# Kernel optimization log

Measured on AMD Instinct MI355X. Metric: run time of the kernel, lower is better.

Reference implementation:

```python
import jax, jax.numpy as jnp
import numpy as np

NUM_CAPSULE = 10
DIM_CAPSULE = 16
NUM_ROUTING = 3
EPS = 1e-7  # tf.keras.backend.epsilon()


def squash(v, axis=-1):
    s2 = jnp.sum(jnp.square(v), axis=axis, keepdims=True)
    scale = s2 / (1.0 + s2) / jnp.sqrt(s2 + EPS)
    return scale * v


def setup_inputs() -> dict:
    key = jax.random.key(0)
    k1, k2 = jax.random.split(key)
    B, in_dim = 16384, 2048
    inputs = jax.random.normal(k1, (B, in_dim), dtype=jnp.float32)
    # glorot-uniform-ish scale for the kernel
    limit = np.sqrt(6.0 / (in_dim + NUM_CAPSULE * DIM_CAPSULE)).astype(np.float32)
    kernel = jax.random.uniform(k2, (in_dim, NUM_CAPSULE * DIM_CAPSULE),
                                dtype=jnp.float32, minval=-limit, maxval=limit)
    return {"inputs": inputs, "kernel": kernel}


def reference(inputs, kernel):
    B = inputs.shape[0]
    # [B, in_dim] @ [in_dim, nc*dc] -> [B, nc, dc]
    inputs_hat = (inputs @ kernel).reshape(B, NUM_CAPSULE, DIM_CAPSULE)
    b = jnp.zeros((B, NUM_CAPSULE, 1), dtype=inputs.dtype)
    outputs = None
    for _ in range(NUM_ROUTING):
        c = jax.nn.softmax(b, axis=1)                      # [B, nc, 1]
        s = jnp.sum(c * inputs_hat, axis=1, keepdims=True)  # [B, 1, dc]
        outputs = squash(s)                                 # [B, 1, dc]
        # matmul(inputs_hat, outputs, transpose_b=True) -> [B, nc, 1]
        b = b + jnp.einsum('bnd,bd->bn', inputs_hat, outputs[:, 0, :])[:, :, None]
    return outputs[:, 0, :]  # [B, dc]
```

## Files before the change

### kernel.cpp

```cpp
#include <hip/hip_runtime.h>

typedef unsigned int u32;
typedef unsigned short u16;
typedef __attribute__((ext_vector_type(8))) __bf16 bf16x8;
typedef __attribute__((ext_vector_type(4))) float f32x4;

#define N_CAP 10
#define D_CAP 16
#define NN 160
#define KK 2048
#define BM 64
#define NSTEPS 64
#define THREADS 704
#define HAT_STRIDE 165
#define BSTEP 20480
#define ATILE 8192
#define NBUF 3

__device__ __align__(16) unsigned char Wpack_g[NSTEPS * BSTEP];

__device__ __forceinline__ u32 pack_hi(float f0, float f1) {
  u32 u0 = __builtin_bit_cast(u32, f0), u1 = __builtin_bit_cast(u32, f1);
  return (u0 >> 16) | (u1 & 0xFFFF0000u);
}
__device__ __forceinline__ float hi_part(float f) {
  u32 u = __builtin_bit_cast(u32, f) & 0xFFFF0000u;
  return __builtin_bit_cast(float, u);
}
union U4B8 { uint4 u; bf16x8 b; };

__device__ __forceinline__ void split2(const float4& x, const float4& y,
                                       bf16x8& h, bf16x8& l) {
  U4B8 hh, ll;
  hh.u.x = pack_hi(x.x, x.y); hh.u.y = pack_hi(x.z, x.w);
  hh.u.z = pack_hi(y.x, y.y); hh.u.w = pack_hi(y.z, y.w);
  float l0 = x.x - hi_part(x.x), l1 = x.y - hi_part(x.y);
  float l2 = x.z - hi_part(x.z), l3 = x.w - hi_part(x.w);
  float l4 = y.x - hi_part(y.x), l5 = y.y - hi_part(y.y);
  float l6 = y.z - hi_part(y.z), l7 = y.w - hi_part(y.w);
  ll.u.x = pack_hi(l0, l1); ll.u.y = pack_hi(l2, l3);
  ll.u.z = pack_hi(l4, l5); ll.u.w = pack_hi(l6, l7);
  h = hh.b; l = ll.b;
}

__device__ __forceinline__ void mfma12(bf16x8 ah0, bf16x8 al0, bf16x8 ah1,
                                       bf16x8 al1, bf16x8 bh0, bf16x8 bh1,
                                       bf16x8 bl0, bf16x8 bl1, f32x4& a00,
                                       f32x4& a01, f32x4& a10, f32x4& a11) {
  a00 = __builtin_amdgcn_mfma_f32_16x16x32_bf16(ah0, bh0, a00, 0, 0, 0);
  a00 = __builtin_amdgcn_mfma_f32_16x16x32_bf16(ah0, bl0, a00, 0, 0, 0);
  a00 = __builtin_amdgcn_mfma_f32_16x16x32_bf16(al0, bh0, a00, 0, 0, 0);
  a01 = __builtin_amdgcn_mfma_f32_16x16x32_bf16(ah0, bh1, a01, 0, 0, 0);
  a01 = __builtin_amdgcn_mfma_f32_16x16x32_bf16(ah0, bl1, a01, 0, 0, 0);
  a01 = __builtin_amdgcn_mfma_f32_16x16x32_bf16(al0, bh1, a01, 0, 0, 0);
  a10 = __builtin_amdgcn_mfma_f32_16x16x32_bf16(ah1, bh0, a10, 0, 0, 0);
  a10 = __builtin_amdgcn_mfma_f32_16x16x32_bf16(ah1, bl0, a10, 0, 0, 0);
  a10 = __builtin_amdgcn_mfma_f32_16x16x32_bf16(al1, bh0, a10, 0, 0, 0);
  a11 = __builtin_amdgcn_mfma_f32_16x16x32_bf16(ah1, bh1, a11, 0, 0, 0);
  a11 = __builtin_amdgcn_mfma_f32_16x16x32_bf16(ah1, bl1, a11, 0, 0, 0);
  a11 = __builtin_amdgcn_mfma_f32_16x16x32_bf16(al1, bh1, a11, 0, 0, 0);
}

__global__ void pack_w(const float* __restrict__ W) {
  const int tid = blockIdx.x * 256 + threadIdx.x;
  if (tid >= NSTEPS * 4 * 5 * 64) return;
  const int lane = tid & 63;
  const int rest = tid >> 6;
  const int wjp = rest % 5;
  const int rest2 = rest / 5;
  const int v = rest2 & 3;
  const int s = rest2 >> 2;
  const int col = 32 * wjp + 16 * (v & 1) + (lane & 15);
  const int kb = 32 * s + 8 * (lane >> 4);
  u32 r[4];
#pragma unroll
  for (int jj = 0; jj < 4; ++jj) {
    float x0 = W[(size_t)(kb + 2 * jj) * NN + col];
    float x1 = W[(size_t)(kb + 2 * jj + 1) * NN + col];
    if (v >= 2) { x0 -= hi_part(x0); x1 -= hi_part(x1); }
    r[jj] = pack_hi(x0, x1);
  }
  uint4 o; o.x = r[0]; o.y = r[1]; o.z = r[2]; o.w = r[3];
  *(uint4*)(Wpack_g + (size_t)tid * 16) = o;
}

#define GLOAD(gp, lp) __builtin_amdgcn_global_load_lds( \
    (const __attribute__((address_space(1))) u32*)(gp), \
    (__attribute__((address_space(3))) u32*)(lp), 16, 0, 0)
#define BARRIER() asm volatile("s_barrier" ::: "memory")

__global__ __launch_bounds__(THREADS, 1) void capsule_fused(
    const float* __restrict__ X, float* __restrict__ out) {
  __shared__ __align__(16) char AsA[NBUF * ATILE];
  __shared__ __align__(16) char AsB[NBUF * BSTEP];
  __shared__ __align__(16) float hat[BM * HAT_STRIDE];

  const int t = threadIdx.x;
  const int rbase = blockIdx.x * BM;
  const int lane = t & 63;
  const int w = t >> 6;

  if (w == 10) {
    const float* g0 = X + (size_t)(rbase + (lane >> 3)) * KK
                        + (size_t)(((lane & 7) ^ (lane >> 3)) * 4);
    const unsigned char* gw0 = Wpack_g + (size_t)lane * 16;
#define STAGE(S, BV) do {                                         \
    const float* ga_ = g0 + (size_t)(S) * 32;                     \
    char* la_ = AsA + (BV) * ATILE;                               \
    GLOAD(ga_,           la_);                                    \
    GLOAD(ga_ +  8 * KK, la_ + 1024);                             \
    GLOAD(ga_ + 16 * KK, la_ + 2048);                             \
    GLOAD(ga_ + 24 * KK, la_ + 3072);                             \
    GLOAD(ga_ + 32 * KK, la_ + 4096);                             \
    GLOAD(ga_ + 40 * KK, la_ + 5120);                             \
    GLOAD(ga_ + 48 * KK, la_ + 6144);                             \
    GLOAD(ga_ + 56 * KK, la_ + 7168);                             \
    const unsigned char* gw_ = gw0 + (size_t)(S) * BSTEP;         \
    char* lw_ = AsB + (BV) * BSTEP;                               \
    _Pragma("unroll")                                             \
    for (int c_ = 0; c_ < 20; ++c_)                               \
      GLOAD(gw_ + c_ * 1024, lw_ + c_ * 1024);                    \
  } while (0)
    STAGE(0, 0);
    STAGE(1, 1);
    asm volatile("s_waitcnt vmcnt(28)" ::: "memory");
    BARRIER();
    int pj = 2;
#pragma unroll 1
    for (int i = 0; i < NSTEPS; ++i) {
      if (i + 2 < NSTEPS) {
        STAGE(i + 2, pj);
        asm volatile("s_waitcnt vmcnt(28)" ::: "memory");
      } else {
        asm volatile("s_waitcnt vmcnt(0)" ::: "memory");
      }
      BARRIER();
      pj = (pj == 2) ? 0 : pj + 1;
    }
#undef STAGE
  } else {
    const int wip = (w >= 5) ? 1 : 0;
    const int wjp = w - 5 * wip;
    const int l15 = lane & 15;
    const int q = lane >> 4;
    const int r0 = 32 * wip + l15;
    const int r1 = r0 + 16;
    const int c0 = 2 * q, c1 = 2 * q + 1;
    const int o00 = (r0 >> 3) * 1024 + (r0 & 7) * 128 + ((c0 ^ (r0 & 7)) << 4);
    const int o01 = (r0 >> 3) * 1024 + (r0 & 7) * 128 + ((c1 ^ (r0 & 7)) << 4);
    const int o10 = (r1 >> 3) * 1024 + (r1 & 7) * 128 + ((c0 ^ (r1 & 7)) << 4);
    const int o11 = (r1 >> 3) * 1024 + (r1 & 7) * 128 + ((c1 ^ (r1 & 7)) << 4);
    const int ob = wjp * 1024 + lane * 16;

    f32x4 acc00 = {0.f,0.f,0.f,0.f}, acc01 = {0.f,0.f,0.f,0.f};
    f32x4 acc10 = {0.f,0.f,0.f,0.f}, acc11 = {0.f,0.f,0.f,0.f};

    BARRIER();
    int ci = 0;
#pragma unroll 1
    for (int i = 0; i < NSTEPS; ++i) {
      const char* ca = AsA + ci * ATILE;
      const char* cbb = AsB + ci * BSTEP + ob;
      bf16x8 bh0 = *(const bf16x8*)(cbb);
      bf16x8 bh1 = *(const bf16x8*)(cbb + 5120);
      bf16x8 bl0 = *(const bf16x8*)(cbb + 10240);
      bf16x8 bl1 = *(const bf16x8*)(cbb + 15360);
      float4 A00 = *(const float4*)(ca + o00);
      float4 A01 = *(const float4*)(ca + o01);
      float4 A10 = *(const float4*)(ca + o10);
      float4 A11 = *(const float4*)(ca + o11);
      bf16x8 ah0, al0, ah1, al1;
      split2(A00, A01, ah0, al0);
      split2(A10, A11, ah1, al1);
      mfma12(ah0, al0, ah1, al1, bh0, bh1, bl0, bl1,
             acc00, acc01, acc10, acc11);
      BARRIER();
      ci = (ci == 2) ? 0 : ci + 1;
    }

#pragma unroll
    for (int r = 0; r < 4; ++r) {
      const int rowb = 32 * wip + 4 * q + r;
      const int colb = 32 * wjp + l15;
      hat[rowb * HAT_STRIDE + colb]             = acc00[r];
      hat[rowb * HAT_STRIDE + colb + 16]        = acc01[r];
      hat[(rowb + 16) * HAT_STRIDE + colb]      = acc10[r];
      hat[(rowb + 16) * HAT_STRIDE + colb + 16] = acc11[r];
    }
  }
  __syncthreads();

  if (t < BM * 8) {
    const int r = t >> 3;
    const int d0 = t & 7;
    float h0[N_CAP], h1[N_CAP];
#pragma unroll
    for (int n = 0; n < N_CAP; ++n) {
      h0[n] = hat[r * HAT_STRIDE + n * D_CAP + d0];
      h1[n] = hat[r * HAT_STRIDE + n * D_CAP + d0 + 8];
    }
    float bb[N_CAP];
#pragma unroll
    for (int n = 0; n < N_CAP; ++n) bb[n] = 0.f;
    float v0 = 0.f, v1 = 0.f;
#pragma unroll
    for (int it = 0; it < 3; ++it) {
      float mx = bb[0];
#pragma unroll
      for (int n = 1; n < N_CAP; ++n) mx = fmaxf(mx, bb[n]);
      float c[N_CAP], se = 0.f;
#pragma unroll
      for (int n = 0; n < N_CAP; ++n) { c[n] = __expf(bb[n] - mx); se += c[n]; }
      const float inv = 1.f / se;
      float s0 = 0.f, s1 = 0.f;
#pragma unroll
      for (int n = 0; n < N_CAP; ++n) { s0 += c[n] * h0[n]; s1 += c[n] * h1[n]; }
      s0 *= inv; s1 *= inv;
      float s2 = s0 * s0 + s1 * s1;
      s2 += __shfl_xor(s2, 1);
      s2 += __shfl_xor(s2, 2);
      s2 += __shfl_xor(s2, 4);
      const float scale = s2 / ((1.f + s2) * sqrtf(s2 + 1e-7f));
      v0 = scale * s0; v1 = scale * s1;
      if (it < 2) {
#pragma unroll
        for (int n = 0; n < N_CAP; ++n) {
          float dd = h0[n] * v0 + h1[n] * v1;
          dd += __shfl_xor(dd, 1);
          dd += __shfl_xor(dd, 2);
          dd += __shfl_xor(dd, 4);
          bb[n] += dd;
        }
      }
    }
    out[(size_t)(rbase + r) * D_CAP + d0] = v0;
    out[(size_t)(rbase + r) * D_CAP + d0 + 8] = v1;
  }
}

extern "C" void kernel_launch(void* const* d_in, const int* in_sizes, int n_in,
                              void* d_out, int out_size, void* d_ws, size_t ws_size,
                              hipStream_t stream) {
  const float* X = (const float*)d_in[0];
  const float* W = (const float*)d_in[1];
  if (n_in >= 2 && in_sizes[0] == KK * NN) {
    X = (const float*)d_in[1];
    W = (const float*)d_in[0];
  }
  (void)d_ws; (void)ws_size; (void)out_size;
  pack_w<<<(NSTEPS * 4 * 5 * 64 + 255) / 256, 256, 0, stream>>>(W);
  capsule_fused<<<16384 / BM, THREADS, 0, stream>>>(X, (float*)d_out);
}
```

Baseline: 208.3 us.

## Prefetch next LDS tile into registers and raise MFMA priority

The consumer waves now double-buffer their operands in registers: the next stage's A and B fragments are read from LDS while the current stage's split and MFMAs run, with an explicit lgkmcnt wait before each barrier. The loader wave's schedule is reshaped so it stays three stages ahead and still never overwrites a slot being read. MFMA blocks are wrapped in s_setprio to favour the matrix work, and the bf16 high-half packing uses a single v_perm. The aim is to hide LDS read latency behind matrix work. The cost is more registers, an unrolled-by-two loop, and tighter barrier bookkeeping between loader and consumers.

Measured after the change: 209.4 us. No clear change (+0.5%).

```diff
diff --git a/kernel.cpp b/kernel.cpp
--- a/kernel.cpp
+++ b/kernel.cpp
@@ -20,8 +20,8 @@
 __device__ __align__(16) unsigned char Wpack_g[NSTEPS * BSTEP];
 
 __device__ __forceinline__ u32 pack_hi(float f0, float f1) {
-  u32 u0 = __builtin_bit_cast(u32, f0), u1 = __builtin_bit_cast(u32, f1);
-  return (u0 >> 16) | (u1 & 0xFFFF0000u);
+  return __builtin_amdgcn_perm(__builtin_bit_cast(u32, f1),
+                               __builtin_bit_cast(u32, f0), 0x07060302u);
 }
 __device__ __forceinline__ float hi_part(float f) {
   u32 u = __builtin_bit_cast(u32, f) & 0xFFFF0000u;
@@ -88,6 +88,7 @@
     (const __attribute__((address_space(1))) u32*)(gp), \
     (__attribute__((address_space(3))) u32*)(lp), 16, 0, 0)
 #define BARRIER() asm volatile("s_barrier" ::: "memory")
+#define LGKM0() asm volatile("s_waitcnt lgkmcnt(0)" ::: "memory")
 
 __global__ __launch_bounds__(THREADS, 1) void capsule_fused(
     const float* __restrict__ X, float* __restrict__ out) {
@@ -123,19 +124,19 @@
   } while (0)
     STAGE(0, 0);
     STAGE(1, 1);
-    asm volatile("s_waitcnt vmcnt(28)" ::: "memory");
-    BARRIER();
-    int pj = 2;
+    asm volatile("s_waitcnt vmcnt(0)" ::: "memory");
+    BARRIER();
+    STAGE(2, 2);
+    BARRIER();
 #pragma unroll 1
     for (int i = 0; i < NSTEPS; ++i) {
-      if (i + 2 < NSTEPS) {
-        STAGE(i + 2, pj);
+      if (i + 3 < NSTEPS) {
+        STAGE(i + 3, i % 3);
         asm volatile("s_waitcnt vmcnt(28)" ::: "memory");
       } else {
         asm volatile("s_waitcnt vmcnt(0)" ::: "memory");
       }
       BARRIER();
-      pj = (pj == 2) ? 0 : pj + 1;
     }
 #undef STAGE
   } else {
@@ -155,28 +156,54 @@
     f32x4 acc00 = {0.f,0.f,0.f,0.f}, acc01 = {0.f,0.f,0.f,0.f};
     f32x4 acc10 = {0.f,0.f,0.f,0.f}, acc11 = {0.f,0.f,0.f,0.f};
 
-    BARRIER();
-    int ci = 0;
+    float4 A00a, A01a, A10a, A11a, A00b, A01b, A10b, A11b;
+    bf16x8 Bh0a, Bh1a, Bl0a, Bl1a, Bh0b, Bh1b, Bl0b, Bl1b;
+
+#define READSET(SFX, SLOT) do {                                   \
+    const char* ca_ = AsA + (SLOT) * ATILE;                       \
+    const char* cb_ = AsB + (SLOT) * BSTEP + ob;                  \
+    A00##SFX = *(const float4*)(ca_ + o00);                       \
+    A01##SFX = *(const float4*)(ca_ + o01);                       \
+    A10##SFX = *(const float4*)(ca_ + o10);                       \
+    A11##SFX = *(const float4*)(ca_ + o11);                       \
+    Bh0##SFX = *(const bf16x8*)(cb_);                             \
+    Bh1##SFX = *(const bf16x8*)(cb_ + 5120);                      \
+    Bl0##SFX = *(const bf16x8*)(cb_ + 10240);                     \
+    Bl1##SFX = *(const bf16x8*)(cb_ + 15360);                     \
+  } while (0)
+
+#define COMPUTE(SFX) do {                                         \
+    bf16x8 ah0, al0, ah1, al1;                                    \
+    split2(A00##SFX, A01##SFX, ah0, al0);                         \
+    split2(A10##SFX, A11##SFX, ah1, al1);                         \
+    __builtin_amdgcn_s_setprio(1);                                \
+    mfma12(ah0, al0, ah1, al1, Bh0##SFX, Bh1##SFX, Bl0##SFX,      \
+           Bl1##SFX, acc00, acc01, acc10, acc11);                 \
+    __builtin_amdgcn_s_setprio(0);                                \
+  } while (0)
+
+    BARRIER();
+    READSET(a, 0);
+    LGKM0();
+    BARRIER();
+    int ni = 1;
 #pragma unroll 1
-    for (int i = 0; i < NSTEPS; ++i) {
-      const char* ca = AsA + ci * ATILE;
-      const char* cbb = AsB + ci * BSTEP + ob;
-      bf16x8 bh0 = *(const bf16x8*)(cbb);
-      bf16x8 bh1 = *(const bf16x8*)(cbb + 5120);
-      bf16x8 bl0 = *(const bf16x8*)(cbb + 10240);
-      bf16x8 bl1 = *(const bf16x8*)(cbb + 15360);
-      float4 A00 = *(const float4*)(ca + o00);
-      float4 A01 = *(const float4*)(ca + o01);
-      float4 A10 = *(const float4*)(ca + o10);
-      float4 A11 = *(const float4*)(ca + o11);
-      bf16x8 ah0, al0, ah1, al1;
-      split2(A00, A01, ah0, al0);
-      split2(A10, A11, ah1, al1);
-      mfma12(ah0, al0, ah1, al1, bh0, bh1, bl0, bl1,
-             acc00, acc01, acc10, acc11);
+    for (int ii = 0; ii < NSTEPS / 2; ++ii) {
+      READSET(b, ni);
+      ni = (ni == 2) ? 0 : ni + 1;
+      COMPUTE(a);
+      LGKM0();
       BARRIER();
-      ci = (ci == 2) ? 0 : ci + 1;
-    }
+      if (ii != NSTEPS / 2 - 1) {
+        READSET(a, ni);
+        ni = (ni == 2) ? 0 : ni + 1;
+      }
+      COMPUTE(b);
+      LGKM0();
+      BARRIER();
+    }
+#undef READSET
+#undef COMPUTE
 
 #pragma unroll
     for (int r = 0; r < 4; ++r) {
```
